# Kernel tuning notes

Hardware: AMD Instinct MI355X
Metric: run time of the kernel (lower is better)

The kernel has to match this reference:

```python
import jax, jax.numpy as jnp
import numpy as np

N_AGENTS = 16384      # number of samples / agents
N_EDGES = 524288      # total relative neighbors (avg degree 32)
FEAT = 4              # relative-neighbor state dim (px, py, vx, vy)
R_AGENT = 0.15        # param.r_agent
BARRIER_MARGIN = 1.2  # hardcoded 1.2 * r_agent in the source


def _glorot(key, shape):
    fan_in = shape[0]
    return jax.random.normal(key, shape, dtype=jnp.float32) / jnp.sqrt(jnp.float32(fan_in))


def setup_inputs() -> dict:
    key = jax.random.key(0)
    ks = jax.random.split(key, 10)
    # Relative positions with |p| in ~[0.7, 3.5] so d - 1.2*r_agent > 0 (physical barrier regime).
    mag = jax.random.uniform(ks[0], (N_EDGES, 2), minval=0.5, maxval=2.5)
    sign = jnp.sign(jax.random.normal(ks[1], (N_EDGES, 2)))
    pos = mag * sign
    vel = 0.1 * jax.random.normal(ks[2], (N_EDGES, 2))
    edge_feats = jnp.concatenate([pos, vel], axis=1)  # [E, 4]
    segment_ids = jnp.sort(jax.random.randint(ks[3], (N_EDGES,), 0, N_AGENTS))
    return {
        "edge_feats": edge_feats,
        "segment_ids": segment_ids,
        "Wp1": _glorot(ks[4], (FEAT, 256)), "bp1": jnp.zeros((256,), jnp.float32),
        "Wp2": _glorot(ks[5], (256, 256)), "bp2": jnp.zeros((256,), jnp.float32),
        "Wp3": _glorot(ks[6], (256, 64)),  "bp3": jnp.zeros((64,), jnp.float32),
        "Wr1": _glorot(ks[7], (64, 256)),  "br1": jnp.zeros((256,), jnp.float32),
        "Wr2": _glorot(ks[8], (256, 256)), "br2": jnp.zeros((256,), jnp.float32),
        "Wr3": _glorot(ks[9], (256, 2)),   "br3": jnp.zeros((2,), jnp.float32),
    }


def reference(edge_feats, segment_ids, Wp1, bp1, Wp2, bp2, Wp3, bp3,
              Wr1, br1, Wr2, br2, Wr3, br3):
    # DeepSet: phi per relative neighbor, sum over each agent's set, rho per agent.
    h = jax.nn.relu(edge_feats @ Wp1 + bp1)          # [E, 256]
    h = jax.nn.relu(h @ Wp2 + bp2)                   # [E, 256]
    h = h @ Wp3 + bp3                                # [E, 64]
    agg = jax.ops.segment_sum(h, segment_ids, num_segments=N_AGENTS)  # [N, 64]
    r = jax.nn.relu(agg @ Wr1 + br1)                 # [N, 256]
    r = jax.nn.relu(r @ Wr2 + br2)                   # [N, 256]
    a_wbarrier = r @ Wr3 + br3                       # [N, 2]

    # Barrier: per edge, -(p/|p|) / (|p| - 1.2*r_agent), scatter-added per agent.
    p = edge_feats[:, :2]                            # [E, 2]
    d = jnp.linalg.norm(p, axis=1, keepdims=True)    # [E, 1]
    contrib = -(p / d) / (d - BARRIER_MARGIN * R_AGENT)  # [E, 2]
    barrier = jax.ops.segment_sum(contrib, segment_ids, num_segments=N_AGENTS)  # [N, 2]

    return a_wbarrier + barrier
```

## Files before the change

### kernel.cpp

```cpp
#include <hip/hip_runtime.h>
#include <hip/hip_bf16.h>

typedef __hip_bfloat16 bf16;
typedef __attribute__((ext_vector_type(8))) short short8;
typedef __attribute__((ext_vector_type(4))) float floatx4;
typedef __attribute__((ext_vector_type(4))) short s16x4;

#define NE 524288
#define NA 16384
#define E  128
#define AG 32
#define S1 260
#define SH3 68

__device__ __forceinline__ float ld(const void* p, long i, int f32) {
    return f32 ? ((const float*)p)[i] : __bfloat162float(((const bf16*)p)[i]);
}
__device__ __forceinline__ short f2bs(float f) {
    bf16 h = __float2bfloat16(f);
    return *(short*)&h;
}
__device__ __forceinline__ float bs2f(short s) {
    union { unsigned u; float f; } c;
    c.u = ((unsigned)(unsigned short)s) << 16;
    return c.f;
}
__device__ __forceinline__ unsigned pk(float a, float b) {
    return ((unsigned)(unsigned short)f2bs(b) << 16) | (unsigned)(unsigned short)f2bs(a);
}

__global__ void prep_weights_kernel(
    const void* __restrict__ Wp1, const void* __restrict__ bp1,
    const void* __restrict__ Wp2, const void* __restrict__ bp2,
    const void* __restrict__ Wp3, const void* __restrict__ bp3,
    const void* __restrict__ Wr1, const void* __restrict__ br1,
    const void* __restrict__ Wr2, const void* __restrict__ br2,
    const void* __restrict__ Wr3, const void* __restrict__ br3,
    short* __restrict__ Wp1P, short* __restrict__ Wp2P, short* __restrict__ Wp3P,
    short* __restrict__ Wr1T,  short* __restrict__ Wr2T,
    float* __restrict__ bp1f, float* __restrict__ bp2f, float* __restrict__ bp3f,
    float* __restrict__ br1f, float* __restrict__ br2f,
    float* __restrict__ Wr3f, float* __restrict__ br3f,
    int* __restrict__ flag)
{
    __shared__ int sflag;
    if (threadIdx.x < 64) {
        const unsigned short* w = (const unsigned short*)Wp2;
        int bad = 0;
        for (int i = threadIdx.x; i < 1024; i += 64) {
            const int e = (w[i] >> 7) & 0xFF;
            if (e >= 131) bad = 1;
        }
        const unsigned long long m = __ballot(bad);
        if (threadIdx.x == 0) {
            sflag = (m != 0ull) ? 1 : 0;
            if (blockIdx.x == 0) *flag = sflag;
        }
    }
    __syncthreads();
    const int f32 = sflag;

    const int stride = gridDim.x * blockDim.x;
    for (int i = blockIdx.x * blockDim.x + threadIdx.x; i < 190018; i += stride) {
        if (i < 65536) {
            const int j = i & 7, lane = (i >> 3) & 63;
            const int nt = (i >> 9) & 1, ks = (i >> 10) & 7, w = (i >> 13) & 7;
            const int n = w * 32 + nt * 16 + (lane & 15);
            const int k = ks * 32 + (lane >> 4) * 8 + j;
            Wp2P[i] = f2bs(ld(Wp2, (long)k * 256 + n, f32));
        } else if (i < 98304) {
            const int ii = i - 65536;
            const int j = ii & 7, lane = (ii >> 3) & 63;
            const int ks = (ii >> 9) & 7, w = (ii >> 12) & 7;
            const int n = (w & 3) * 16 + (lane & 15);
            const int k = ks * 32 + (lane >> 4) * 8 + j;
            Wp3P[ii] = f2bs(ld(Wp3, (long)k * 64 + n, f32));
        } else if (i < 106496) {
            const int ii = i - 98304;
            const int j = ii & 7, lane = (ii >> 3) & 63;
            const int nt = (ii >> 9) & 1, w = (ii >> 10) & 7;
            const int n = w * 32 + nt * 16 + (lane & 15);
            const int k = (lane >> 4) * 8 + j;
            Wp1P[ii] = (k < 4) ? f2bs(ld(Wp1, (long)k * 256 + n, f32)) : (short)0;
        } else if (i < 122880) {
            const int jj = i - 106496, n = jj >> 6, k = jj & 63;
            Wr1T[jj] = f2bs(ld(Wr1, (long)k * 256 + n, f32));
        } else if (i < 188416) {
            const int jj = i - 122880, n = jj >> 8, k = jj & 255;
            Wr2T[jj] = f2bs(ld(Wr2, (long)k * 256 + n, f32));
        } else if (i < 188672) { bp1f[i - 188416] = ld(bp1, i - 188416, f32); }
        else if (i < 188928) { bp2f[i - 188672] = ld(bp2, i - 188672, f32); }
        else if (i < 188992) { bp3f[i - 188928] = ld(bp3, i - 188928, f32); }
        else if (i < 189248) { br1f[i - 188992] = ld(br1, i - 188992, f32); }
        else if (i < 189504) { br2f[i - 189248] = ld(br2, i - 189248, f32); }
        else if (i < 190016) { Wr3f[i - 189504] = ld(Wr3, i - 189504, f32); }
        else                 { br3f[i - 190016] = ld(br3, i - 190016, f32); }
    }
}

__global__ __launch_bounds__(512, 4) void edge_mlp_kernel(
    const void* __restrict__ ef, const int* __restrict__ ids,
    const short* __restrict__ Wp1P, const float* __restrict__ bp1f,
    const short* __restrict__ Wp2P, const float* __restrict__ bp2f,
    const short* __restrict__ Wp3P, const float* __restrict__ bp3f,
    float* __restrict__ agg, float* __restrict__ bar,
    const int* __restrict__ flag)
{
    __shared__ __align__(16) short hs[E * S1];
    __shared__ float cb[E][2];
    __shared__ int   sid[E];

    const int t = threadIdx.x;
    const long e0 = (long)blockIdx.x * E;
    const int f32 = *flag;
    const int wave = t >> 6, lane = t & 63, quad = lane >> 4, ln = lane & 15;
    const int nw = wave * 32;

    if (t < E) {
        sid[t] = ids[e0 + t];
        const float px = ld(ef, (e0 + t) * 4 + 0, f32);
        const float py = ld(ef, (e0 + t) * 4 + 1, f32);
        const float d = sqrtf(px * px + py * py);
        const float inv = 1.0f / (d * (d - 0.18f));
        cb[t][0] = -px * inv;
        cb[t][1] = -py * inv;
    }

    {
        short8 b[8];
        #pragma unroll
        for (int mt = 0; mt < 8; ++mt) {
            short8 v = {};
            if (quad == 0) {
                const long e = e0 + mt * 16 + ln;
                if (f32) {
                    const float4 x = ((const float4*)ef)[e];
                    v[0] = f2bs(x.x); v[1] = f2bs(x.y); v[2] = f2bs(x.z); v[3] = f2bs(x.w);
                } else {
                    const int2 x = ((const int2*)ef)[e];
                    v[0] = (short)(x.x & 0xffff); v[1] = (short)((unsigned)x.x >> 16);
                    v[2] = (short)(x.y & 0xffff); v[3] = (short)((unsigned)x.y >> 16);
                }
            }
            b[mt] = v;
        }
        floatx4 acc[8][2];
        #pragma unroll
        for (int nt = 0; nt < 2; ++nt) {
            const float4 bv = *(const float4*)&bp1f[nw + nt * 16 + quad * 4];
            const floatx4 bi = { bv.x, bv.y, bv.z, bv.w };
            #pragma unroll
            for (int mt = 0; mt < 8; ++mt) acc[mt][nt] = bi;
        }
        #pragma unroll
        for (int nt = 0; nt < 2; ++nt) {
            const short8 a = *(const short8*)&Wp1P[((wave * 2 + nt) * 64 + lane) * 8];
            #pragma unroll
            for (int mt = 0; mt < 8; ++mt)
                acc[mt][nt] = __builtin_amdgcn_mfma_f32_16x16x32_bf16(a, b[mt], acc[mt][nt], 0, 0, 0);
        }
        #pragma unroll
        for (int mt = 0; mt < 8; ++mt)
            #pragma unroll
            for (int nt = 0; nt < 2; ++nt) {
                const floatx4 v = acc[mt][nt];
                uint2 w;
                w.x = pk(fmaxf(v[0], 0.f), fmaxf(v[1], 0.f));
                w.y = pk(fmaxf(v[2], 0.f), fmaxf(v[3], 0.f));
                *(uint2*)&hs[(mt * 16 + ln) * S1 + nw + nt * 16 + quad * 4] = w;
            }
    }
    __syncthreads();

    {
        floatx4 acc[8][2];
        #pragma unroll
        for (int nt = 0; nt < 2; ++nt) {
            const float4 bv = *(const float4*)&bp2f[nw + nt * 16 + quad * 4];
            const floatx4 bi = { bv.x, bv.y, bv.z, bv.w };
            #pragma unroll
            for (int mt = 0; mt < 8; ++mt) acc[mt][nt] = bi;
        }
        short8 wcur[2], wnxt[2];
        #pragma unroll
        for (int nt = 0; nt < 2; ++nt)
            wcur[nt] = *(const short8*)&Wp2P[(((wave * 8 + 0) * 2 + nt) * 64 + lane) * 8];
        #pragma unroll
        for (int ks = 0; ks < 8; ++ks) {
            if (ks < 7) {
                #pragma unroll
                for (int nt = 0; nt < 2; ++nt)
                    wnxt[nt] = *(const short8*)&Wp2P[(((wave * 8 + ks + 1) * 2 + nt) * 64 + lane) * 8];
            }
            #pragma unroll
            for (int mh = 0; mh < 2; ++mh) {
                short8 b[4];
                #pragma unroll
                for (int m4 = 0; m4 < 4; ++m4)
                    b[m4] = *(const short8*)&hs[((mh * 4 + m4) * 16 + ln) * S1 + ks * 32 + quad * 8];
                #pragma unroll
                for (int m4 = 0; m4 < 4; ++m4)
                    #pragma unroll
                    for (int nt = 0; nt < 2; ++nt)
                        acc[mh * 4 + m4][nt] = __builtin_amdgcn_mfma_f32_16x16x32_bf16(wcur[nt], b[m4], acc[mh * 4 + m4][nt], 0, 0, 0);
            }
            #pragma unroll
            for (int nt = 0; nt < 2; ++nt) wcur[nt] = wnxt[nt];
        }
        __syncthreads();
        #pragma unroll
        for (int mt = 0; mt < 8; ++mt)
            #pragma unroll
            for (int nt = 0; nt < 2; ++nt) {
                const floatx4 v = acc[mt][nt];
                uint2 w;
                w.x = pk(fmaxf(v[0], 0.f), fmaxf(v[1], 0.f));
                w.y = pk(fmaxf(v[2], 0.f), fmaxf(v[3], 0.f));
                *(uint2*)&hs[(mt * 16 + ln) * S1 + nw + nt * 16 + quad * 4] = w;
            }
    }
    __syncthreads();

    const int me = (wave >> 2) * 64;
    const int fb = (wave & 3) * 16;
    floatx4 acc3[4];
    {
        const float4 bv = *(const float4*)&bp3f[fb + quad * 4];
        const floatx4 bi = { bv.x, bv.y, bv.z, bv.w };
        #pragma unroll
        for (int mt = 0; mt < 4; ++mt) acc3[mt] = bi;
        short8 w3 = *(const short8*)&Wp3P[((wave * 8 + 0) * 64 + lane) * 8];
        #pragma unroll
        for (int ks = 0; ks < 8; ++ks) {
            short8 wn = w3;
            if (ks < 7)
                wn = *(const short8*)&Wp3P[((wave * 8 + ks + 1) * 64 + lane) * 8];
            #pragma unroll
            for (int mt = 0; mt < 4; ++mt) {
                const short8 b = *(const short8*)&hs[(me + mt * 16 + ln) * S1 + ks * 32 + quad * 8];
                acc3[mt] = __builtin_amdgcn_mfma_f32_16x16x32_bf16(w3, b, acc3[mt], 0, 0, 0);
            }
            w3 = wn;
        }
    }
    __syncthreads();
    float* h3f = (float*)hs;
    #pragma unroll
    for (int mt = 0; mt < 4; ++mt) {
        float4 v = { acc3[mt][0], acc3[mt][1], acc3[mt][2], acc3[mt][3] };
        *(float4*)&h3f[(me + mt * 16 + ln) * SH3 + fb + quad * 4] = v;
    }
    __syncthreads();

    {
        const int w0 = wave * 16;
        const int f = lane;
        int cur = sid[w0];
        float local = h3f[w0 * SH3 + f];
        #pragma unroll
        for (int e = 1; e < 16; ++e) {
            const int id = sid[w0 + e];
            const float v = h3f[(w0 + e) * SH3 + f];
            if (id == cur) local += v;
            else { atomicAdd(&agg[(long)cur * 64 + f], local); cur = id; local = v; }
        }
        atomicAdd(&agg[(long)cur * 64 + f], local);

        if (lane < 2) {
            int c2 = sid[w0];
            float l2 = cb[w0][lane];
            #pragma unroll
            for (int e = 1; e < 16; ++e) {
                const int id = sid[w0 + e];
                const float v = cb[w0 + e][lane];
                if (id == c2) l2 += v;
                else { atomicAdd(&bar[c2 * 2 + lane], l2); c2 = id; l2 = v; }
            }
            atomicAdd(&bar[c2 * 2 + lane], l2);
        }
    }
}

__global__ __launch_bounds__(256, 2) void agent_mlp_kernel(
    const float* __restrict__ agg, const float* __restrict__ bar,
    const short* __restrict__ Wr1T, const float* __restrict__ br1f,
    const short* __restrict__ Wr2T, const float* __restrict__ br2f,
    const float* __restrict__ Wr3f, const float* __restrict__ br3f,
    void* __restrict__ out, const int* __restrict__ flag)
{
    __shared__ __align__(16) short ha[AG * 68];
    __shared__ __align__(16) short hs[AG * S1];
    __shared__ float part[8][AG][2];

    const int t = threadIdx.x;
    const int a0 = blockIdx.x * AG;
    const int f32 = *flag;
    const int wave = t >> 6, lane = t & 63, quad = lane >> 4, ln = lane & 15;
    const int nb = wave * 64;

    #pragma unroll
    for (int i = 0; i < 2; ++i) {
        const float4 x = ((const float4*)agg)[(long)blockIdx.x * 512 + i * 256 + t];
        const int idx4 = (i * 256 + t) * 4;
        s16x4 v = { f2bs(x.x), f2bs(x.y), f2bs(x.z), f2bs(x.w) };
        *(s16x4*)&ha[(idx4 >> 6) * 68 + (idx4 & 63)] = v;
    }
    __syncthreads();

    {
        floatx4 acc[2][4];
        #pragma unroll
        for (int nt = 0; nt < 4; ++nt) {
            const float4 bv = *(const float4*)&br1f[nb + nt * 16 + quad * 4];
            const floatx4 bi = { bv.x, bv.y, bv.z, bv.w };
            #pragma unroll
            for (int mt = 0; mt < 2; ++mt) acc[mt][nt] = bi;
        }
        #pragma unroll
        for (int ks = 0; ks < 2; ++ks) {
            short8 b[2], a[4];
            #pragma unroll
            for (int mt = 0; mt < 2; ++mt)
                b[mt] = *(const short8*)&ha[(mt * 16 + ln) * 68 + ks * 32 + quad * 8];
            #pragma unroll
            for (int nt = 0; nt < 4; ++nt)
                a[nt] = *(const short8*)&Wr1T[(nb + nt * 16 + ln) * 64 + ks * 32 + quad * 8];
            #pragma unroll
            for (int mt = 0; mt < 2; ++mt)
                #pragma unroll
                for (int nt = 0; nt < 4; ++nt)
                    acc[mt][nt] = __builtin_amdgcn_mfma_f32_16x16x32_bf16(a[nt], b[mt], acc[mt][nt], 0, 0, 0);
        }
        #pragma unroll
        for (int mt = 0; mt < 2; ++mt)
            #pragma unroll
            for (int nt = 0; nt < 4; ++nt) {
                const floatx4 v = acc[mt][nt];
                uint2 w;
                w.x = pk(fmaxf(v[0], 0.f), fmaxf(v[1], 0.f));
                w.y = pk(fmaxf(v[2], 0.f), fmaxf(v[3], 0.f));
                *(uint2*)&hs[(mt * 16 + ln) * S1 + nb + nt * 16 + quad * 4] = w;
            }
    }
    __syncthreads();

    {
        floatx4 acc[2][4];
        #pragma unroll
        for (int nt = 0; nt < 4; ++nt) {
            const float4 bv = *(const float4*)&br2f[nb + nt * 16 + quad * 4];
            const floatx4 bi = { bv.x, bv.y, bv.z, bv.w };
            #pragma unroll
            for (int mt = 0; mt < 2; ++mt) acc[mt][nt] = bi;
        }
        short8 wcur[4], wnxt[4];
        #pragma unroll
        for (int nt = 0; nt < 4; ++nt)
            wcur[nt] = *(const short8*)&Wr2T[(nb + nt * 16 + ln) * 256 + quad * 8];
        #pragma unroll
        for (int ks = 0; ks < 8; ++ks) {
            if (ks < 7) {
                #pragma unroll
                for (int nt = 0; nt < 4; ++nt)
                    wnxt[nt] = *(const short8*)&Wr2T[(nb + nt * 16 + ln) * 256 + (ks + 1) * 32 + quad * 8];
            }
            short8 b[2];
            #pragma unroll
            for (int mt = 0; mt < 2; ++mt)
                b[mt] = *(const short8*)&hs[(mt * 16 + ln) * S1 + ks * 32 + quad * 8];
            #pragma unroll
            for (int mt = 0; mt < 2; ++mt)
                #pragma unroll
                for (int nt = 0; nt < 4; ++nt)
                    acc[mt][nt] = __builtin_amdgcn_mfma_f32_16x16x32_bf16(wcur[nt], b[mt], acc[mt][nt], 0, 0, 0);
            #pragma unroll
            for (int nt = 0; nt < 4; ++nt) wcur[nt] = wnxt[nt];
        }
        __syncthreads();
        #pragma unroll
        for (int mt = 0; mt < 2; ++mt)
            #pragma unroll
            for (int nt = 0; nt < 4; ++nt) {
                const floatx4 v = acc[mt][nt];
                uint2 w;
                w.x = pk(fmaxf(v[0], 0.f), fmaxf(v[1], 0.f));
                w.y = pk(fmaxf(v[2], 0.f), fmaxf(v[3], 0.f));
                *(uint2*)&hs[(mt * 16 + ln) * S1 + nb + nt * 16 + quad * 4] = w;
            }
    }
    __syncthreads();

    {
        const int m = t & 31;
        const int p = t >> 5;
        float v0 = 0.f, v1 = 0.f;
        #pragma unroll
        for (int kk = 0; kk < 4; ++kk) {
            const int k0 = p * 32 + kk * 8;
            const short8 h = *(const short8*)&hs[m * S1 + k0];
            #pragma unroll
            for (int j = 0; j < 8; ++j) {
                const float hv = bs2f(h[j]);
                v0 = fmaf(hv, Wr3f[(k0 + j) * 2 + 0], v0);
                v1 = fmaf(hv, Wr3f[(k0 + j) * 2 + 1], v1);
            }
        }
        part[p][m][0] = v0;
        part[p][m][1] = v1;
    }
    __syncthreads();
    if (t < 64) {
        const int m = t >> 1, o = t & 1;
        float s = br3f[o] + bar[(long)(a0 + m) * 2 + o];
        #pragma unroll
        for (int p = 0; p < 8; ++p) s += part[p][m][o];
        if (f32) ((float*)out)[(a0 + m) * 2 + o] = s;
        else     ((bf16*)out)[(a0 + m) * 2 + o] = __float2bfloat16(s);
    }
}

extern "C" void kernel_launch(void* const* d_in, const int* in_sizes, int n_in,
                              void* d_out, int out_size, void* d_ws, size_t ws_size,
                              hipStream_t stream)
{
    (void)in_sizes; (void)n_in; (void)out_size;

    const void* ef  = d_in[0];
    const int*  ids = (const int*)d_in[1];

    char* p = (char*)d_ws;
    int*   flag  = (int*)p;        p += 256;
    float* agg   = (float*)p;      p += (size_t)NA * 64 * 4;
    float* bar   = (float*)p;      p += (size_t)NA * 2 * 4;
    short* Wp1P  = (short*)p;      p += 8192 * 2;
    short* Wp2P  = (short*)p;      p += 65536 * 2;
    short* Wp3P  = (short*)p;      p += 32768 * 2;
    short* Wr1T  = (short*)p;      p += 16384 * 2;
    short* Wr2T  = (short*)p;      p += 65536 * 2;
    float* bp1f  = (float*)p;      p += 256 * 4;
    float* bp2f  = (float*)p;      p += 256 * 4;
    float* bp3f  = (float*)p;      p += 64 * 4;
    float* br1f  = (float*)p;      p += 256 * 4;
    float* br2f  = (float*)p;      p += 256 * 4;
    float* Wr3f  = (float*)p;      p += 512 * 4;
    float* br3f  = (float*)p;      p += 256;
    const size_t required = (size_t)(p - (char*)d_ws);
    if (ws_size < required) return;

    hipMemsetAsync(agg, 0, ((size_t)NA * 64 + (size_t)NA * 2) * 4, stream);
    prep_weights_kernel<<<64, 256, 0, stream>>>(
        d_in[2], d_in[3], d_in[4], d_in[5], d_in[6], d_in[7],
        d_in[8], d_in[9], d_in[10], d_in[11], d_in[12], d_in[13],
        Wp1P, Wp2P, Wp3P, Wr1T, Wr2T,
        bp1f, bp2f, bp3f, br1f, br2f, Wr3f, br3f, flag);
    edge_mlp_kernel<<<NE / E, 512, 0, stream>>>(
        ef, ids, Wp1P, bp1f, Wp2P, bp2f, Wp3P, bp3f, agg, bar, flag);
    agent_mlp_kernel<<<NA / AG, 256, 0, stream>>>(
        agg, bar, Wr1T, br1f, Wr2T, br2f, Wr3f, br3f, d_out, flag);
}
```

Measured before the change: 204.7 us.

## Pre-swizzle agent MLP weights, shrink agent tile, hoist loads, remap edge blocks

Agent MLP weights are now pre-packed into the per-lane MFMA fragment layout, as the edge MLP already does, so weight loads become contiguous 16-byte vectors. The agent tile shrinks from 32 to 16 agents per block with higher occupancy bounds. In the edge kernel, weight and bias loads are hoisted to the kernel start, blocks are remapped in a strided order, and the MFMA bursts are wrapped in s_setprio. The agent-kernel changes trade per-block weight reuse for more blocks and better latency hiding, and the hoisted loads add register pressure.

```diff
diff --git a/kernel.cpp b/kernel.cpp
--- a/kernel.cpp
+++ b/kernel.cpp
@@ -9,7 +9,7 @@
 #define NE 524288
 #define NA 16384
 #define E  128
-#define AG 32
+#define AG 16
 #define S1 260
 #define SH3 68
 
@@ -37,7 +37,7 @@
     const void* __restrict__ Wr2, const void* __restrict__ br2,
     const void* __restrict__ Wr3, const void* __restrict__ br3,
     short* __restrict__ Wp1P, short* __restrict__ Wp2P, short* __restrict__ Wp3P,
-    short* __restrict__ Wr1T,  short* __restrict__ Wr2T,
+    short* __restrict__ Wr1P,  short* __restrict__ Wr2P,
     float* __restrict__ bp1f, float* __restrict__ bp2f, float* __restrict__ bp3f,
     float* __restrict__ br1f, float* __restrict__ br2f,
     float* __restrict__ Wr3f, float* __restrict__ br3f,
@@ -83,11 +83,19 @@
             const int k = (lane >> 4) * 8 + j;
             Wp1P[ii] = (k < 4) ? f2bs(ld(Wp1, (long)k * 256 + n, f32)) : (short)0;
         } else if (i < 122880) {
-            const int jj = i - 106496, n = jj >> 6, k = jj & 63;
-            Wr1T[jj] = f2bs(ld(Wr1, (long)k * 256 + n, f32));
+            const int ii = i - 106496;
+            const int j = ii & 7, lane = (ii >> 3) & 63;
+            const int nt = (ii >> 9) & 3, ks = (ii >> 11) & 1, w = (ii >> 12) & 3;
+            const int n = w * 64 + nt * 16 + (lane & 15);
+            const int k = ks * 32 + (lane >> 4) * 8 + j;
+            Wr1P[ii] = f2bs(ld(Wr1, (long)k * 256 + n, f32));
         } else if (i < 188416) {
-            const int jj = i - 122880, n = jj >> 8, k = jj & 255;
-            Wr2T[jj] = f2bs(ld(Wr2, (long)k * 256 + n, f32));
+            const int ii = i - 122880;
+            const int j = ii & 7, lane = (ii >> 3) & 63;
+            const int nt = (ii >> 9) & 3, ks = (ii >> 11) & 7, w = (ii >> 14) & 3;
+            const int n = w * 64 + nt * 16 + (lane & 15);
+            const int k = ks * 32 + (lane >> 4) * 8 + j;
+            Wr2P[ii] = f2bs(ld(Wr2, (long)k * 256 + n, f32));
         } else if (i < 188672) { bp1f[i - 188416] = ld(bp1, i - 188416, f32); }
         else if (i < 188928) { bp2f[i - 188672] = ld(bp2, i - 188672, f32); }
         else if (i < 188992) { bp3f[i - 188928] = ld(bp3, i - 188928, f32); }
@@ -111,10 +119,27 @@
     __shared__ int   sid[E];
 
     const int t = threadIdx.x;
-    const long e0 = (long)blockIdx.x * E;
+    const int bid = blockIdx.x;
+    const int wg = (bid & 7) * ((NE / E) >> 3) + (bid >> 3);
+    const long e0 = (long)wg * E;
     const int f32 = *flag;
     const int wave = t >> 6, lane = t & 63, quad = lane >> 4, ln = lane & 15;
     const int nw = wave * 32;
+    const int me = (wave >> 2) * 64;
+    const int fb = (wave & 3) * 16;
+
+    short8 wcur[2], wnxt[2];
+    #pragma unroll
+    for (int nt = 0; nt < 2; ++nt)
+        wcur[nt] = *(const short8*)&Wp2P[(((wave * 8 + 0) * 2 + nt) * 64 + lane) * 8];
+    float4 b1v[2], b2v[2];
+    #pragma unroll
+    for (int nt = 0; nt < 2; ++nt) {
+        b1v[nt] = *(const float4*)&bp1f[nw + nt * 16 + quad * 4];
+        b2v[nt] = *(const float4*)&bp2f[nw + nt * 16 + quad * 4];
+    }
+    short8 w3;
+    float4 b3v;
 
     if (t < E) {
         sid[t] = ids[e0 + t];
@@ -147,8 +172,7 @@
         floatx4 acc[8][2];
         #pragma unroll
         for (int nt = 0; nt < 2; ++nt) {
-            const float4 bv = *(const float4*)&bp1f[nw + nt * 16 + quad * 4];
-            const floatx4 bi = { bv.x, bv.y, bv.z, bv.w };
+            const floatx4 bi = { b1v[nt].x, b1v[nt].y, b1v[nt].z, b1v[nt].w };
             #pragma unroll
             for (int mt = 0; mt < 8; ++mt) acc[mt][nt] = bi;
         }
@@ -176,15 +200,10 @@
         floatx4 acc[8][2];
         #pragma unroll
         for (int nt = 0; nt < 2; ++nt) {
-            const float4 bv = *(const float4*)&bp2f[nw + nt * 16 + quad * 4];
-            const floatx4 bi = { bv.x, bv.y, bv.z, bv.w };
+            const floatx4 bi = { b2v[nt].x, b2v[nt].y, b2v[nt].z, b2v[nt].w };
             #pragma unroll
             for (int mt = 0; mt < 8; ++mt) acc[mt][nt] = bi;
         }
-        short8 wcur[2], wnxt[2];
-        #pragma unroll
-        for (int nt = 0; nt < 2; ++nt)
-            wcur[nt] = *(const short8*)&Wp2P[(((wave * 8 + 0) * 2 + nt) * 64 + lane) * 8];
         #pragma unroll
         for (int ks = 0; ks < 8; ++ks) {
             if (ks < 7) {
@@ -198,15 +217,19 @@
                 #pragma unroll
                 for (int m4 = 0; m4 < 4; ++m4)
                     b[m4] = *(const short8*)&hs[((mh * 4 + m4) * 16 + ln) * S1 + ks * 32 + quad * 8];
+                __builtin_amdgcn_s_setprio(1);
                 #pragma unroll
                 for (int m4 = 0; m4 < 4; ++m4)
                     #pragma unroll
                     for (int nt = 0; nt < 2; ++nt)
                         acc[mh * 4 + m4][nt] = __builtin_amdgcn_mfma_f32_16x16x32_bf16(wcur[nt], b[m4], acc[mh * 4 + m4][nt], 0, 0, 0);
+                __builtin_amdgcn_s_setprio(0);
             }
             #pragma unroll
             for (int nt = 0; nt < 2; ++nt) wcur[nt] = wnxt[nt];
         }
+        w3  = *(const short8*)&Wp3P[((wave * 8 + 0) * 64 + lane) * 8];
+        b3v = *(const float4*)&bp3f[fb + quad * 4];
         __syncthreads();
         #pragma unroll
         for (int mt = 0; mt < 8; ++mt)
@@ -221,25 +244,25 @@
     }
     __syncthreads();
 
-    const int me = (wave >> 2) * 64;
-    const int fb = (wave & 3) * 16;
     floatx4 acc3[4];
     {
-        const float4 bv = *(const float4*)&bp3f[fb + quad * 4];
-        const floatx4 bi = { bv.x, bv.y, bv.z, bv.w };
+        const floatx4 bi = { b3v.x, b3v.y, b3v.z, b3v.w };
         #pragma unroll
         for (int mt = 0; mt < 4; ++mt) acc3[mt] = bi;
-        short8 w3 = *(const short8*)&Wp3P[((wave * 8 + 0) * 64 + lane) * 8];
         #pragma unroll
         for (int ks = 0; ks < 8; ++ks) {
             short8 wn = w3;
             if (ks < 7)
                 wn = *(const short8*)&Wp3P[((wave * 8 + ks + 1) * 64 + lane) * 8];
-            #pragma unroll
-            for (int mt = 0; mt < 4; ++mt) {
-                const short8 b = *(const short8*)&hs[(me + mt * 16 + ln) * S1 + ks * 32 + quad * 8];
-                acc3[mt] = __builtin_amdgcn_mfma_f32_16x16x32_bf16(w3, b, acc3[mt], 0, 0, 0);
-            }
+            short8 b[4];
+            #pragma unroll
+            for (int mt = 0; mt < 4; ++mt)
+                b[mt] = *(const short8*)&hs[(me + mt * 16 + ln) * S1 + ks * 32 + quad * 8];
+            __builtin_amdgcn_s_setprio(1);
+            #pragma unroll
+            for (int mt = 0; mt < 4; ++mt)
+                acc3[mt] = __builtin_amdgcn_mfma_f32_16x16x32_bf16(w3, b[mt], acc3[mt], 0, 0, 0);
+            __builtin_amdgcn_s_setprio(0);
             w3 = wn;
         }
     }
@@ -281,16 +304,16 @@
     }
 }
 
-__global__ __launch_bounds__(256, 2) void agent_mlp_kernel(
+__global__ __launch_bounds__(256, 4) void agent_mlp_kernel(
     const float* __restrict__ agg, const float* __restrict__ bar,
-    const short* __restrict__ Wr1T, const float* __restrict__ br1f,
-    const short* __restrict__ Wr2T, const float* __restrict__ br2f,
+    const short* __restrict__ Wr1P, const float* __restrict__ br1f,
+    const short* __restrict__ Wr2P, const float* __restrict__ br2f,
     const float* __restrict__ Wr3f, const float* __restrict__ br3f,
     void* __restrict__ out, const int* __restrict__ flag)
 {
     __shared__ __align__(16) short ha[AG * 68];
     __shared__ __align__(16) short hs[AG * S1];
-    __shared__ float part[8][AG][2];
+    __shared__ float part[16][AG][2];
 
     const int t = threadIdx.x;
     const int a0 = blockIdx.x * AG;
@@ -298,105 +321,98 @@
     const int wave = t >> 6, lane = t & 63, quad = lane >> 4, ln = lane & 15;
     const int nb = wave * 64;
 
+    float4 r1b[4], r2b[4];
     #pragma unroll
-    for (int i = 0; i < 2; ++i) {
-        const float4 x = ((const float4*)agg)[(long)blockIdx.x * 512 + i * 256 + t];
-        const int idx4 = (i * 256 + t) * 4;
+    for (int nt = 0; nt < 4; ++nt) {
+        r1b[nt] = *(const float4*)&br1f[nb + nt * 16 + quad * 4];
+        r2b[nt] = *(const float4*)&br2f[nb + nt * 16 + quad * 4];
+    }
+    short8 a1[4], wcur[4], wnxt[4];
+    #pragma unroll
+    for (int nt = 0; nt < 4; ++nt) {
+        a1[nt]   = *(const short8*)&Wr1P[(((wave * 2 + 0) * 4 + nt) * 64 + lane) * 8];
+        wcur[nt] = *(const short8*)&Wr2P[(((wave * 8 + 0) * 4 + nt) * 64 + lane) * 8];
+    }
+    float barv = 0.f;
+    if (t < 2 * AG) barv = bar[(long)a0 * 2 + t];
+
+    {
+        const float4 x = ((const float4*)agg)[(long)blockIdx.x * 256 + t];
         s16x4 v = { f2bs(x.x), f2bs(x.y), f2bs(x.z), f2bs(x.w) };
-        *(s16x4*)&ha[(idx4 >> 6) * 68 + (idx4 & 63)] = v;
-    }
-    __syncthreads();
-
-    {
-        floatx4 acc[2][4];
+        *(s16x4*)&ha[(t >> 4) * 68 + (t & 15) * 4] = v;
+    }
+    __syncthreads();
+
+    {
+        floatx4 acc[4];
+        #pragma unroll
+        for (int nt = 0; nt < 4; ++nt)
+            acc[nt] = (floatx4){ r1b[nt].x, r1b[nt].y, r1b[nt].z, r1b[nt].w };
+        #pragma unroll
+        for (int ks = 0; ks < 2; ++ks) {
+            const short8 b = *(const short8*)&ha[ln * 68 + ks * 32 + quad * 8];
+            short8 a[4];
+            #pragma unroll
+            for (int nt = 0; nt < 4; ++nt)
+                a[nt] = (ks == 0) ? a1[nt]
+                      : *(const short8*)&Wr1P[(((wave * 2 + ks) * 4 + nt) * 64 + lane) * 8];
+            __builtin_amdgcn_s_setprio(1);
+            #pragma unroll
+            for (int nt = 0; nt < 4; ++nt)
+                acc[nt] = __builtin_amdgcn_mfma_f32_16x16x32_bf16(a[nt], b, acc[nt], 0, 0, 0);
+            __builtin_amdgcn_s_setprio(0);
+        }
         #pragma unroll
         for (int nt = 0; nt < 4; ++nt) {
-            const float4 bv = *(const float4*)&br1f[nb + nt * 16 + quad * 4];
-            const floatx4 bi = { bv.x, bv.y, bv.z, bv.w };
-            #pragma unroll
-            for (int mt = 0; mt < 2; ++mt) acc[mt][nt] = bi;
-        }
-        #pragma unroll
-        for (int ks = 0; ks < 2; ++ks) {
-            short8 b[2], a[4];
-            #pragma unroll
-            for (int mt = 0; mt < 2; ++mt)
-                b[mt] = *(const short8*)&ha[(mt * 16 + ln) * 68 + ks * 32 + quad * 8];
-            #pragma unroll
-            for (int nt = 0; nt < 4; ++nt)
-                a[nt] = *(const short8*)&Wr1T[(nb + nt * 16 + ln) * 64 + ks * 32 + quad * 8];
-            #pragma unroll
-            for (int mt = 0; mt < 2; ++mt)
-                #pragma unroll
-                for (int nt = 0; nt < 4; ++nt)
-                    acc[mt][nt] = __builtin_amdgcn_mfma_f32_16x16x32_bf16(a[nt], b[mt], acc[mt][nt], 0, 0, 0);
-        }
-        #pragma unroll
-        for (int mt = 0; mt < 2; ++mt)
-            #pragma unroll
-            for (int nt = 0; nt < 4; ++nt) {
-                const floatx4 v = acc[mt][nt];
-                uint2 w;
-                w.x = pk(fmaxf(v[0], 0.f), fmaxf(v[1], 0.f));
-                w.y = pk(fmaxf(v[2], 0.f), fmaxf(v[3], 0.f));
-                *(uint2*)&hs[(mt * 16 + ln) * S1 + nb + nt * 16 + quad * 4] = w;
-            }
-    }
-    __syncthreads();
-
-    {
-        floatx4 acc[2][4];
-        #pragma unroll
-        for (int nt = 0; nt < 4; ++nt) {
-            const float4 bv = *(const float4*)&br2f[nb + nt * 16 + quad * 4];
-            const floatx4 bi = { bv.x, bv.y, bv.z, bv.w };
-            #pragma unroll
-            for (int mt = 0; mt < 2; ++mt) acc[mt][nt] = bi;
-        }
-        short8 wcur[4], wnxt[4];
+            const floatx4 v = acc[nt];
+            uint2 w;
+            w.x = pk(fmaxf(v[0], 0.f), fmaxf(v[1], 0.f));
+            w.y = pk(fmaxf(v[2], 0.f), fmaxf(v[3], 0.f));
+            *(uint2*)&hs[ln * S1 + nb + nt * 16 + quad * 4] = w;
+        }
+    }
+    __syncthreads();
+
+    {
+        floatx4 acc[4];
         #pragma unroll
         for (int nt = 0; nt < 4; ++nt)
-            wcur[nt] = *(const short8*)&Wr2T[(nb + nt * 16 + ln) * 256 + quad * 8];
+            acc[nt] = (floatx4){ r2b[nt].x, r2b[nt].y, r2b[nt].z, r2b[nt].w };
         #pragma unroll
         for (int ks = 0; ks < 8; ++ks) {
             if (ks < 7) {
                 #pragma unroll
                 for (int nt = 0; nt < 4; ++nt)
-                    wnxt[nt] = *(const short8*)&Wr2T[(nb + nt * 16 + ln) * 256 + (ks + 1) * 32 + quad * 8];
-            }
-            short8 b[2];
-            #pragma unroll
-            for (int mt = 0; mt < 2; ++mt)
-                b[mt] = *(const short8*)&hs[(mt * 16 + ln) * S1 + ks * 32 + quad * 8];
-            #pragma unroll
-            for (int mt = 0; mt < 2; ++mt)
-                #pragma unroll
-                for (int nt = 0; nt < 4; ++nt)
-                    acc[mt][nt] = __builtin_amdgcn_mfma_f32_16x16x32_bf16(wcur[nt], b[mt], acc[mt][nt], 0, 0, 0);
+                    wnxt[nt] = *(const short8*)&Wr2P[(((wave * 8 + ks + 1) * 4 + nt) * 64 + lane) * 8];
+            }
+            const short8 b = *(const short8*)&hs[ln * S1 + ks * 32 + quad * 8];
+            __builtin_amdgcn_s_setprio(1);
+            #pragma unroll
+            for (int nt = 0; nt < 4; ++nt)
+                acc[nt] = __builtin_amdgcn_mfma_f32_16x16x32_bf16(wcur[nt], b, acc[nt], 0, 0, 0);
+            __builtin_amdgcn_s_setprio(0);
             #pragma unroll
             for (int nt = 0; nt < 4; ++nt) wcur[nt] = wnxt[nt];
         }
         __syncthreads();
         #pragma unroll
-        for (int mt = 0; mt < 2; ++mt)
-            #pragma unroll
-            for (int nt = 0; nt < 4; ++nt) {
-                const floatx4 v = acc[mt][nt];
-                uint2 w;
-                w.x = pk(fmaxf(v[0], 0.f), fmaxf(v[1], 0.f));
-                w.y = pk(fmaxf(v[2], 0.f), fmaxf(v[3], 0.f));
-                *(uint2*)&hs[(mt * 16 + ln) * S1 + nb + nt * 16 + quad * 4] = w;
-            }
-    }
-    __syncthreads();
-
-    {
-        const int m = t & 31;
-        const int p = t >> 5;
+        for (int nt = 0; nt < 4; ++nt) {
+            const floatx4 v = acc[nt];
+            uint2 w;
+            w.x = pk(fmaxf(v[0], 0.f), fmaxf(v[1], 0.f));
+            w.y = pk(fmaxf(v[2], 0.f), fmaxf(v[3], 0.f));
+            *(uint2*)&hs[ln * S1 + nb + nt * 16 + quad * 4] = w;
+        }
+    }
+    __syncthreads();
+
+    {
+        const int m = t & 15;
+        const int p = t >> 4;
         float v0 = 0.f, v1 = 0.f;
         #pragma unroll
-        for (int kk = 0; kk < 4; ++kk) {
-            const int k0 = p * 32 + kk * 8;
+        for (int kk = 0; kk < 2; ++kk) {
+            const int k0 = p * 16 + kk * 8;
             const short8 h = *(const short8*)&hs[m * S1 + k0];
             #pragma unroll
             for (int j = 0; j < 8; ++j) {
@@ -409,13 +425,13 @@
         part[p][m][1] = v1;
     }
     __syncthreads();
-    if (t < 64) {
+    if (t < 2 * AG) {
         const int m = t >> 1, o = t & 1;
-        float s = br3f[o] + bar[(long)(a0 + m) * 2 + o];
-        #pragma unroll
-        for (int p = 0; p < 8; ++p) s += part[p][m][o];
-        if (f32) ((float*)out)[(a0 + m) * 2 + o] = s;
-        else     ((bf16*)out)[(a0 + m) * 2 + o] = __float2bfloat16(s);
+        float s = br3f[o] + barv;
+        #pragma unroll
+        for (int p = 0; p < 16; ++p) s += part[p][m][o];
+        if (f32) ((float*)out)[a0 * 2 + t] = s;
+        else     ((bf16*)out)[a0 * 2 + t] = __float2bfloat16(s);
     }
 }
 
@@ -435,8 +451,8 @@
     short* Wp1P  = (short*)p;      p += 8192 * 2;
     short* Wp2P  = (short*)p;      p += 65536 * 2;
     short* Wp3P  = (short*)p;      p += 32768 * 2;
-    short* Wr1T  = (short*)p;      p += 16384 * 2;
-    short* Wr2T  = (short*)p;      p += 65536 * 2;
+    short* Wr1P  = (short*)p;      p += 16384 * 2;
+    short* Wr2P  = (short*)p;      p += 65536 * 2;
     float* bp1f  = (float*)p;      p += 256 * 4;
     float* bp2f  = (float*)p;      p += 256 * 4;
     float* bp3f  = (float*)p;      p += 64 * 4;
@@ -451,10 +467,10 @@
     prep_weights_kernel<<<64, 256, 0, stream>>>(
         d_in[2], d_in[3], d_in[4], d_in[5], d_in[6], d_in[7],
         d_in[8], d_in[9], d_in[10], d_in[11], d_in[12], d_in[13],
-        Wp1P, Wp2P, Wp3P, Wr1T, Wr2T,
+        Wp1P, Wp2P, Wp3P, Wr1P, Wr2P,
         bp1f, bp2f, bp3f, br1f, br2f, Wr3f, br3f, flag);
     edge_mlp_kernel<<<NE / E, 512, 0, stream>>>(
         ef, ids, Wp1P, bp1f, Wp2P, bp2f, Wp3P, bp3f, agg, bar, flag);
     agent_mlp_kernel<<<NA / AG, 256, 0, stream>>>(
-        agg, bar, Wr1T, br1f, Wr2T, br2f, Wr3f, br3f, d_out, flag);
-}
+        agg, bar, Wr1P, br1f, Wr2P, br2f, Wr3f, br3f, d_out, flag);
+}
```

Measured after the change: 204.7 us. About the same (-0.0%).
